# Kernel tuning notes

Measured on AMD Instinct MI355X. Metric: run time of the kernel, lower is better.

Reference implementation:

```python
import math
import jax, jax.numpy as jnp
import numpy as np

D = 512
H = 8
HD = D // H
FF = 2048
EPS = 1e-5


def _layernorm(x, gamma, beta):
    mean = jnp.mean(x, axis=-1, keepdims=True)
    var = jnp.mean((x - mean) ** 2, axis=-1, keepdims=True)
    return gamma * (x - mean) / jnp.sqrt(var + EPS) + beta


def _attention(q, k, v, mask):
    # q,k,v: [B,H,Sq/Sk,hd]; mask: [B,Sq,Sk] additive, broadcast over heads
    scale = 1.0 / math.sqrt(q.shape[-1])
    scores = jnp.einsum('bhqd,bhkd->bhqk', q, k) * scale
    scores = scores + mask[:, None, :, :]
    probs = jax.nn.softmax(scores, axis=-1)
    return jnp.einsum('bhqk,bhkd->bhqd', probs, v)


def setup_inputs() -> dict:
    key = jax.random.key(0)
    ks = jax.random.split(key, 20)
    B, S_ENC, S_DEC = 256, 512, 64
    s = 0.02
    inp = {
        'x': jax.random.normal(ks[0], (B, S_ENC, D), jnp.float32),
        'y': jax.random.normal(ks[1], (B, S_DEC, D), jnp.float32),
        'mask': jnp.zeros((B, S_DEC, S_DEC), jnp.float32),
        'mask2': jnp.zeros((B, S_DEC, S_ENC), jnp.float32),
        # self-attention params
        'qkv_w': jax.random.normal(ks[2], (D, 3 * D), jnp.float32) * s,
        'qkv_b': jnp.zeros((3 * D,), jnp.float32),
        'sa_out_w': jax.random.normal(ks[3], (D, D), jnp.float32) * s,
        'sa_out_b': jnp.zeros((D,), jnp.float32),
        # cross-attention params
        'q_w': jax.random.normal(ks[4], (D, D), jnp.float32) * s,
        'q_b': jnp.zeros((D,), jnp.float32),
        'kv_w': jax.random.normal(ks[5], (D, 2 * D), jnp.float32) * s,
        'kv_b': jnp.zeros((2 * D,), jnp.float32),
        'ca_out_w': jax.random.normal(ks[6], (D, D), jnp.float32) * s,
        'ca_out_b': jnp.zeros((D,), jnp.float32),
        # ffn params
        'l1_w': jax.random.normal(ks[7], (D, FF), jnp.float32) * s,
        'l1_b': jnp.zeros((FF,), jnp.float32),
        'l2_w': jax.random.normal(ks[8], (FF, D), jnp.float32) * s,
        'l2_b': jnp.zeros((D,), jnp.float32),
        # layernorm params
        'g1': jnp.ones((D,), jnp.float32), 'b1': jnp.zeros((D,), jnp.float32),
        'g2': jnp.ones((D,), jnp.float32), 'b2': jnp.zeros((D,), jnp.float32),
        'g3': jnp.ones((D,), jnp.float32), 'b3': jnp.zeros((D,), jnp.float32),
    }
    return inp


def reference(x, y, mask, mask2, qkv_w, qkv_b, sa_out_w, sa_out_b,
              q_w, q_b, kv_w, kv_b, ca_out_w, ca_out_b,
              l1_w, l1_b, l2_w, l2_b, g1, b1, g2, b2, g3, b3):
    B, Sd, _ = y.shape
    Se = x.shape[1]

    # --- self attention (post-norm, dropout is identity at eval) ---
    resid = y
    qkv = y @ qkv_w + qkv_b                     # [B,Sd,3D]
    qkv = qkv.reshape(B, Sd, H, 3 * HD).transpose(0, 2, 1, 3)
    q, k, v = jnp.split(qkv, 3, axis=-1)        # each [B,H,Sd,hd]
    vals = _attention(q, k, v, mask)
    vals = vals.transpose(0, 2, 1, 3).reshape(B, Sd, D)
    y = vals @ sa_out_w + sa_out_b
    y = _layernorm(y + resid, g1, b1)

    # --- cross attention: kv from encoder x, q from decoder y ---
    resid = y
    kv = x @ kv_w + kv_b                        # [B,Se,2D]
    kv = kv.reshape(B, Se, H, 2 * HD).transpose(0, 2, 1, 3)
    k, v = jnp.split(kv, 2, axis=-1)            # each [B,H,Se,hd]
    q = (y @ q_w + q_b).reshape(B, Sd, H, HD).transpose(0, 2, 1, 3)
    vals = _attention(q, k, v, mask2)
    vals = vals.transpose(0, 2, 1, 3).reshape(B, Sd, D)
    y = vals @ ca_out_w + ca_out_b
    y = _layernorm(y + resid, g2, b2)

    # --- feed forward ---
    resid = y
    h = jax.nn.relu(y @ l1_w + l1_b)
    y = h @ l2_w + l2_b
    y = _layernorm(y + resid, g3, b3)
    return y
```

## Files before the change

### kernel.cpp

```cpp
#include <hip/hip_runtime.h>
#include <hip/hip_bf16.h>
#include <stdint.h>


#define SDEC 64
#define SENC 512
#define DMODEL 512
#define FFDIM 2048

typedef __bf16 bf16x8 __attribute__((ext_vector_type(8)));
typedef float  f32x4  __attribute__((ext_vector_type(4)));

static __device__ __forceinline__ float bf2f(unsigned short u) {
  union { unsigned int i; float f; } w; w.i = ((unsigned int)u) << 16; return w.f;
}
static __device__ __forceinline__ unsigned short f2bf(float f) {
  union { float f; unsigned int i; } w; w.f = f;
  unsigned int u = w.i;
  return (unsigned short)((u + 0x7fffu + ((u >> 16) & 1u)) >> 16);
}

static __device__ __forceinline__ void gl_lds16(const unsigned short* g, unsigned short* l) {
  __builtin_amdgcn_global_load_lds(
      (const __attribute__((address_space(1))) unsigned int*)g,
      (__attribute__((address_space(3))) unsigned int*)l,
      16, 0, 0);
}

__global__ __launch_bounds__(256)
void cvt_f32_bf16(const float* __restrict__ in, unsigned short* __restrict__ out, size_t n8)
{
  size_t i = (size_t)blockIdx.x * blockDim.x + threadIdx.x;
  const size_t stride = (size_t)gridDim.x * blockDim.x;
  for (; i < n8; i += stride) {
    const float* p = in + i * 8;
    float4 a = *(const float4*)p, b = *(const float4*)(p + 4);
    union { unsigned short s[8]; uint4 v; } u;
    u.s[0] = f2bf(a.x); u.s[1] = f2bf(a.y); u.s[2] = f2bf(a.z); u.s[3] = f2bf(a.w);
    u.s[4] = f2bf(b.x); u.s[5] = f2bf(b.y); u.s[6] = f2bf(b.z); u.s[7] = f2bf(b.w);
    *(uint4*)(out + i * 8) = u.v;
  }
}

template<int RELU>
__global__ __launch_bounds__(256, 2)
void gemm_kernel(const unsigned short* __restrict__ A, const unsigned short* __restrict__ Bt,
                 const float* __restrict__ bias, unsigned short* __restrict__ C,
                 int M, int N, int K)
{
  __shared__ unsigned short sh[3 * 8192];
  const int tid = threadIdx.x;

  const int gx   = gridDim.x;
  const int nwg  = gx * gridDim.y;
  const int orig = blockIdx.y * gx + blockIdx.x;
  const int wg   = (orig & 7) * (nwg >> 3) + (orig >> 3);
  const int row0 = (wg / gx) * 128;
  const int col0 = (wg % gx) * 128;

  const int w = tid >> 6, lane = tid & 63;
  const int wm = w >> 1, wn = w & 1;
  const int gr = lane >> 2;
  const int gc = ((lane & 3) ^ ((lane >> 4) & 3)) * 8;

  auto STAGE = [&](int k0, int buf) {
    unsigned short* as = sh + buf * 8192;
    unsigned short* bs = as + 4096;
    #pragma unroll
    for (int i = 0; i < 2; ++i) {
      const int rbase = w * 32 + i * 16;
      gl_lds16(A  + (size_t)(row0 + rbase + gr) * K + (k0 + gc), as + rbase * 32);
      gl_lds16(Bt + (size_t)(col0 + rbase + gr) * K + (k0 + gc), bs + rbase * 32);
    }
  };

  f32x4 acc[4][4];
  #pragma unroll
  for (int i = 0; i < 4; ++i)
    #pragma unroll
    for (int j = 0; j < 4; ++j)
      acc[i][j] = (f32x4){0.f, 0.f, 0.f, 0.f};

  const int fr  = lane & 15;
  const int fks = ((lane >> 4) ^ (fr >> 2)) * 8;

  auto COMPUTE = [&](int buf) {
    const unsigned short* as = sh + buf * 8192;
    const unsigned short* bs = as + 4096;
    bf16x8 af[4], bfr[4];
    #pragma unroll
    for (int mi = 0; mi < 4; ++mi)
      af[mi] = *(const bf16x8*)&as[(wm * 64 + mi * 16 + fr) * 32 + fks];
    #pragma unroll
    for (int ni = 0; ni < 4; ++ni)
      bfr[ni] = *(const bf16x8*)&bs[(wn * 64 + ni * 16 + fr) * 32 + fks];
    __builtin_amdgcn_s_setprio(1);
    #pragma unroll
    for (int mi = 0; mi < 4; ++mi)
      #pragma unroll
      for (int ni = 0; ni < 4; ++ni)
        acc[mi][ni] = __builtin_amdgcn_mfma_f32_16x16x32_bf16(af[mi], bfr[ni], acc[mi][ni], 0, 0, 0);
    __builtin_amdgcn_s_setprio(0);
  };

  const int NT = K >> 5;
  STAGE(0, 0);
  STAGE(32, 1);
  int bc = 0, bn = 2;
  for (int t = 0; t < NT - 2; ++t) {
    STAGE((t + 2) << 5, bn);
    asm volatile("s_waitcnt vmcnt(8)" ::: "memory");
    __builtin_amdgcn_s_barrier();
    asm volatile("" ::: "memory");
    COMPUTE(bc);
    asm volatile("" ::: "memory");
    __builtin_amdgcn_s_barrier();
    bc = (bc + 1 == 3) ? 0 : bc + 1;
    bn = (bn + 1 == 3) ? 0 : bn + 1;
  }
  asm volatile("s_waitcnt vmcnt(4)" ::: "memory");
  __builtin_amdgcn_s_barrier();
  asm volatile("" ::: "memory");
  COMPUTE(bc);
  asm volatile("" ::: "memory");
  __builtin_amdgcn_s_barrier();
  bc = (bc + 1 == 3) ? 0 : bc + 1;
  asm volatile("s_waitcnt vmcnt(0)" ::: "memory");
  __builtin_amdgcn_s_barrier();
  asm volatile("" ::: "memory");
  COMPUTE(bc);
  asm volatile("" ::: "memory");
  __builtin_amdgcn_s_barrier();

  {
    const int fq = lane >> 4;
    #pragma unroll
    for (int ni = 0; ni < 4; ++ni) {
      const int c = wn * 64 + ni * 16 + fr;
      const float bv = bias ? bias[col0 + c] : 0.f;
      #pragma unroll
      for (int mi = 0; mi < 4; ++mi) {
        #pragma unroll
        for (int t = 0; t < 4; ++t) {
          const int r = wm * 64 + mi * 16 + fq * 4 + t;
          float v = acc[mi][ni][t] + bv;
          if (RELU) v = fmaxf(v, 0.f);
          sh[r * 128 + c] = f2bf(v);
        }
      }
    }
    __syncthreads();
    const int rr = tid >> 4;
    const int cc = (tid & 15) * 8;
    #pragma unroll
    for (int p = 0; p < 8; ++p) {
      const int r = p * 16 + rr;
      *(uint4*)(C + (size_t)(row0 + r) * N + col0 + cc) = *(const uint4*)&sh[r * 128 + cc];
    }
  }
}

__global__ __launch_bounds__(256, 2)
void attn_mfma(const unsigned short* __restrict__ qbuf, int qstride, int qmul,
               const unsigned short* __restrict__ kvbuf, int kvstride, int kmul, int kadd,
               int tokmul, int Skv, const float* __restrict__ mask,
               unsigned short* __restrict__ vals, float scale)
{
  __shared__ unsigned short Qs[64 * 72];
  __shared__ unsigned short Ks[64 * 72];
  __shared__ unsigned short Vt[64 * 72];
  __shared__ unsigned short Ps[64 * 72];

  const int nwg  = gridDim.x * gridDim.y;
  const int orig = blockIdx.y * gridDim.x + blockIdx.x;
  const int wg   = (orig & 7) * (nwg >> 3) + (orig >> 3);
  const int h = wg & 7, b = wg >> 3;

  const int tid = threadIdx.x;
  const int w = tid >> 6, lane = tid & 63;
  const int srow = tid >> 2;
  const int sc0 = (tid & 3) * 16;

  {
    const unsigned short* qg = qbuf + (size_t)(b * 64 + srow) * qstride + h * qmul + sc0;
    *(uint4*)&Qs[srow * 72 + sc0]     = *(const uint4*)qg;
    *(uint4*)&Qs[srow * 72 + sc0 + 8] = *(const uint4*)(qg + 8);
  }

  const int fr = lane & 15;
  const int fg = lane >> 4;
  const int orow = fg * 4;

  float mstate[4], lstate[4];
  f32x4 oacc[4];
  #pragma unroll
  for (int t = 0; t < 4; ++t) { mstate[t] = -1e30f; lstate[t] = 0.f; }
  #pragma unroll
  for (int ni = 0; ni < 4; ++ni) oacc[ni] = (f32x4){0.f, 0.f, 0.f, 0.f};

  for (int j0 = 0; j0 < Skv; j0 += 64) {
    __syncthreads();
    {
      const unsigned short* kg = kvbuf + (size_t)(b * tokmul + j0 + srow) * kvstride
                                 + h * kmul + kadd + sc0;
      *(uint4*)&Ks[srow * 72 + sc0]     = *(const uint4*)kg;
      *(uint4*)&Ks[srow * 72 + sc0 + 8] = *(const uint4*)(kg + 8);
      const unsigned short* vg = kg + 64;
      uint4 v0 = *(const uint4*)vg;
      uint4 v1 = *(const uint4*)(vg + 8);
      const unsigned short* vsp = (const unsigned short*)&v0;
      #pragma unroll
      for (int jj = 0; jj < 8; ++jj) Vt[(sc0 + jj) * 72 + srow] = vsp[jj];
      vsp = (const unsigned short*)&v1;
      #pragma unroll
      for (int jj = 0; jj < 8; ++jj) Vt[(sc0 + 8 + jj) * 72 + srow] = vsp[jj];
    }
    __syncthreads();

    f32x4 s[4];
    #pragma unroll
    for (int ni = 0; ni < 4; ++ni) s[ni] = (f32x4){0.f, 0.f, 0.f, 0.f};
    #pragma unroll
    for (int ks = 0; ks < 2; ++ks) {
      bf16x8 aq = *(const bf16x8*)&Qs[(w * 16 + fr) * 72 + ks * 32 + fg * 8];
      #pragma unroll
      for (int ni = 0; ni < 4; ++ni) {
        bf16x8 bk = *(const bf16x8*)&Ks[(ni * 16 + fr) * 72 + ks * 32 + fg * 8];
        s[ni] = __builtin_amdgcn_mfma_f32_16x16x32_bf16(aq, bk, s[ni], 0, 0, 0);
      }
    }

    #pragma unroll
    for (int t = 0; t < 4; ++t) {
      const int grow = w * 16 + orow + t;
      const float* mrow = mask + ((size_t)b * 64 + grow) * Skv + j0;
      float sv[4];
      float tmax = -1e30f;
      #pragma unroll
      for (int ni = 0; ni < 4; ++ni) {
        sv[ni] = s[ni][t] * scale + mrow[ni * 16 + fr];
        tmax = fmaxf(tmax, sv[ni]);
      }
      #pragma unroll
      for (int off = 1; off < 16; off <<= 1) tmax = fmaxf(tmax, __shfl_xor(tmax, off));
      const float mn = fmaxf(mstate[t], tmax);
      const float fscl = __expf(mstate[t] - mn);
      mstate[t] = mn;
      float psum = 0.f;
      #pragma unroll
      for (int ni = 0; ni < 4; ++ni) {
        float p = __expf(sv[ni] - mn);
        psum += p;
        Ps[grow * 72 + ni * 16 + fr] = f2bf(p);
      }
      #pragma unroll
      for (int off = 1; off < 16; off <<= 1) psum += __shfl_xor(psum, off);
      lstate[t] = lstate[t] * fscl + psum;
      #pragma unroll
      for (int ni = 0; ni < 4; ++ni) oacc[ni][t] *= fscl;
    }
    __syncthreads();

    #pragma unroll
    for (int ks = 0; ks < 2; ++ks) {
      bf16x8 pa = *(const bf16x8*)&Ps[(w * 16 + fr) * 72 + ks * 32 + fg * 8];
      #pragma unroll
      for (int ni = 0; ni < 4; ++ni) {
        bf16x8 vb = *(const bf16x8*)&Vt[(ni * 16 + fr) * 72 + ks * 32 + fg * 8];
        oacc[ni] = __builtin_amdgcn_mfma_f32_16x16x32_bf16(pa, vb, oacc[ni], 0, 0, 0);
      }
    }
  }

  #pragma unroll
  for (int t = 0; t < 4; ++t) {
    const int grow = w * 16 + orow + t;
    const float inv = 1.f / lstate[t];
    unsigned short* og = vals + (size_t)(b * 64 + grow) * DMODEL + h * 64;
    #pragma unroll
    for (int ni = 0; ni < 4; ++ni)
      og[ni * 16 + fr] = f2bf(oacc[ni][t] * inv);
  }
}

__global__ __launch_bounds__(256)
void ln_kernel(const unsigned short* __restrict__ proj16, const float* __restrict__ resid32,
               const unsigned short* __restrict__ resid16,
               const float* __restrict__ gamma, const float* __restrict__ beta,
               unsigned short* __restrict__ out16, float* __restrict__ out32)
{
  const int w = threadIdx.x >> 6, lane = threadIdx.x & 63;
  const size_t r = (size_t)blockIdx.x * 4 + w;
  const int d0 = lane * 8;

  float x[8];
  {
    uint4 u = *(const uint4*)(proj16 + r * DMODEL + d0);
    const unsigned short* s = (const unsigned short*)&u;
    #pragma unroll
    for (int j = 0; j < 8; ++j) x[j] = bf2f(s[j]);
  }
  if (resid32) {
    const float* p = resid32 + r * DMODEL + d0;
    float4 a = *(const float4*)p, b = *(const float4*)(p + 4);
    x[0] += a.x; x[1] += a.y; x[2] += a.z; x[3] += a.w;
    x[4] += b.x; x[5] += b.y; x[6] += b.z; x[7] += b.w;
  } else {
    uint4 u = *(const uint4*)(resid16 + r * DMODEL + d0);
    const unsigned short* s = (const unsigned short*)&u;
    #pragma unroll
    for (int j = 0; j < 8; ++j) x[j] += bf2f(s[j]);
  }

  float sum = 0.f;
  #pragma unroll
  for (int j = 0; j < 8; ++j) sum += x[j];
  #pragma unroll
  for (int off = 32; off > 0; off >>= 1) sum += __shfl_xor(sum, off);
  const float mean = sum * (1.f / DMODEL);

  float vs = 0.f;
  #pragma unroll
  for (int j = 0; j < 8; ++j) { float t = x[j] - mean; vs += t * t; }
  #pragma unroll
  for (int off = 32; off > 0; off >>= 1) vs += __shfl_xor(vs, off);
  const float rstd = rsqrtf(vs * (1.f / DMODEL) + 1e-5f);

  float4 g0 = *(const float4*)(gamma + d0), g1 = *(const float4*)(gamma + d0 + 4);
  float4 b0 = *(const float4*)(beta + d0),  b1 = *(const float4*)(beta + d0 + 4);
  const float g[8]  = {g0.x, g0.y, g0.z, g0.w, g1.x, g1.y, g1.z, g1.w};
  const float bb[8] = {b0.x, b0.y, b0.z, b0.w, b1.x, b1.y, b1.z, b1.w};
  float y[8];
  #pragma unroll
  for (int j = 0; j < 8; ++j) y[j] = g[j] * (x[j] - mean) * rstd + bb[j];

  if (out16) {
    union { unsigned short s[8]; uint4 v; } p;
    #pragma unroll
    for (int j = 0; j < 8; ++j) p.s[j] = f2bf(y[j]);
    *(uint4*)(out16 + r * DMODEL + d0) = p.v;
  }
  if (out32) {
    float* o = out32 + r * DMODEL + d0;
    *(float4*)o       = (float4){y[0], y[1], y[2], y[3]};
    *(float4*)(o + 4) = (float4){y[4], y[5], y[6], y[7]};
  }
}

__global__ __launch_bounds__(256)
void transpose_cvt(const float* __restrict__ W, unsigned short* __restrict__ Wt,
                   int K, int N)
{
  __shared__ float tile[32][33];
  const int tx = threadIdx.x, ty = threadIdx.y;
  const int n = blockIdx.x * 32 + tx;
  #pragma unroll
  for (int rr = 0; rr < 4; ++rr) {
    const int k = blockIdx.y * 32 + ty + rr * 8;
    tile[ty + rr * 8][tx] = W[(size_t)k * N + n];
  }
  __syncthreads();
  const int k2 = blockIdx.y * 32 + tx;
  #pragma unroll
  for (int rr = 0; rr < 4; ++rr) {
    const int n2 = blockIdx.x * 32 + ty + rr * 8;
    Wt[(size_t)n2 * K + k2] = f2bf(tile[tx][ty + rr * 8]);
  }
}

extern "C" void kernel_launch(void* const* d_in, const int* in_sizes, int n_in,
                              void* d_out, int out_size, void* d_ws, size_t ws_size,
                              hipStream_t stream)
{
  const float* x        = (const float*)d_in[0];
  const float* y        = (const float*)d_in[1];
  const float* mask     = (const float*)d_in[2];
  const float* mask2    = (const float*)d_in[3];
  const float* qkv_w    = (const float*)d_in[4];
  const float* qkv_b    = (const float*)d_in[5];
  const float* sa_out_w = (const float*)d_in[6];
  const float* sa_out_b = (const float*)d_in[7];
  const float* q_w      = (const float*)d_in[8];
  const float* q_b      = (const float*)d_in[9];
  const float* kv_w     = (const float*)d_in[10];
  const float* kv_b     = (const float*)d_in[11];
  const float* ca_out_w = (const float*)d_in[12];
  const float* ca_out_b = (const float*)d_in[13];
  const float* l1_w     = (const float*)d_in[14];
  const float* l1_b     = (const float*)d_in[15];
  const float* l2_w     = (const float*)d_in[16];
  const float* l2_b     = (const float*)d_in[17];
  const float* g1 = (const float*)d_in[18];
  const float* b1 = (const float*)d_in[19];
  const float* g2 = (const float*)d_in[20];
  const float* b2 = (const float*)d_in[21];
  const float* g3 = (const float*)d_in[22];
  const float* b3 = (const float*)d_in[23];

  const int B  = in_sizes[1] / (SDEC * DMODEL);
  const int M  = B * SDEC;
  const int ME = B * SENC;

  char* ws = (char*)d_ws;
  size_t off = 0;
  auto alloc = [&](size_t bytes) -> char* {
    char* p = ws + off;
    off += (bytes + 255) & ~(size_t)255;
    return p;
  };
  unsigned short* qkv_wt = (unsigned short*)alloc((size_t)1536 * 512 * 2);
  unsigned short* sa_wt  = (unsigned short*)alloc((size_t)512 * 512 * 2);
  unsigned short* q_wt   = (unsigned short*)alloc((size_t)512 * 512 * 2);
  unsigned short* kv_wt  = (unsigned short*)alloc((size_t)1024 * 512 * 2);
  unsigned short* ca_wt  = (unsigned short*)alloc((size_t)512 * 512 * 2);
  unsigned short* l1_wt  = (unsigned short*)alloc((size_t)2048 * 512 * 2);
  unsigned short* l2_wt  = (unsigned short*)alloc((size_t)512 * 2048 * 2);
  unsigned short* kvb    = (unsigned short*)alloc((size_t)ME * 1024 * 2);
  char*           xreg   = alloc((size_t)ME * 512 * 2);
  unsigned short* xb     = (unsigned short*)xreg;
  unsigned short* qkvb   = (unsigned short*)xreg;
  unsigned short* qb     = (unsigned short*)xreg;
  unsigned short* y2b    = (unsigned short*)(xreg + (size_t)16777216);
  unsigned short* valsb  = (unsigned short*)(xreg + (size_t)50331648);
  unsigned short* proj   = (unsigned short*)(xreg + (size_t)67108864);
  unsigned short* y1b    = (unsigned short*)(xreg + (size_t)100663296);
  unsigned short* yb     = (unsigned short*)(xreg + (size_t)117440512);
  unsigned short* hb     = kvb;
  (void)ws_size; (void)n_in; (void)out_size;

  dim3 tb(32, 8);
  transpose_cvt<<<dim3(1536 / 32, 512 / 32), tb, 0, stream>>>(qkv_w, qkv_wt, 512, 1536);
  transpose_cvt<<<dim3(512 / 32, 512 / 32), tb, 0, stream>>>(sa_out_w, sa_wt, 512, 512);
  transpose_cvt<<<dim3(512 / 32, 512 / 32), tb, 0, stream>>>(q_w, q_wt, 512, 512);
  transpose_cvt<<<dim3(1024 / 32, 512 / 32), tb, 0, stream>>>(kv_w, kv_wt, 512, 1024);
  transpose_cvt<<<dim3(512 / 32, 512 / 32), tb, 0, stream>>>(ca_out_w, ca_wt, 512, 512);
  transpose_cvt<<<dim3(2048 / 32, 512 / 32), tb, 0, stream>>>(l1_w, l1_wt, 512, 2048);
  transpose_cvt<<<dim3(512 / 32, 2048 / 32), tb, 0, stream>>>(l2_w, l2_wt, 2048, 512);

  const float scale = 0.125f;

  cvt_f32_bf16<<<4096, 256, 0, stream>>>(x, xb, (size_t)ME * 512 / 8);
  gemm_kernel<0><<<dim3(1024 / 128, ME / 128), 256, 0, stream>>>(xb, kv_wt, kv_b, kvb, ME, 1024, 512);

  cvt_f32_bf16<<<4096, 256, 0, stream>>>(y, yb, (size_t)M * 512 / 8);
  gemm_kernel<0><<<dim3(1536 / 128, M / 128), 256, 0, stream>>>(yb, qkv_wt, qkv_b, qkvb, M, 1536, 512);
  attn_mfma<<<dim3(8, B), 256, 0, stream>>>(qkvb, 1536, 192, qkvb, 1536, 192, 64, SDEC, SDEC, mask, valsb, scale);
  gemm_kernel<0><<<dim3(512 / 128, M / 128), 256, 0, stream>>>(valsb, sa_wt, sa_out_b, proj, M, 512, 512);
  ln_kernel<<<M / 4, 256, 0, stream>>>(proj, y, nullptr, g1, b1, y1b, nullptr);

  gemm_kernel<0><<<dim3(512 / 128, M / 128), 256, 0, stream>>>(y1b, q_wt, q_b, qb, M, 512, 512);
  attn_mfma<<<dim3(8, B), 256, 0, stream>>>(qb, 512, 64, kvb, 1024, 128, 0, SENC, SENC, mask2, valsb, scale);
  gemm_kernel<0><<<dim3(512 / 128, M / 128), 256, 0, stream>>>(valsb, ca_wt, ca_out_b, proj, M, 512, 512);
  ln_kernel<<<M / 4, 256, 0, stream>>>(proj, nullptr, y1b, g2, b2, y2b, nullptr);

  gemm_kernel<1><<<dim3(2048 / 128, M / 128), 256, 0, stream>>>(y2b, l1_wt, l1_b, hb, M, 2048, 512);
  gemm_kernel<0><<<dim3(512 / 128, M / 128), 256, 0, stream>>>(hb, l2_wt, l2_b, proj, M, 512, 2048);
  ln_kernel<<<M / 4, 256, 0, stream>>>(proj, nullptr, y2b, g3, b3, nullptr, (float*)d_out);
}
```

Baseline: 628.4 us.

## Fuse fp32-to-bf16 input conversion into GEMM A-tile loading, double-buffer GEMM

Removes the separate fp32→bf16 conversion kernels for the encoder and decoder inputs. A new GEMM variant loads fp32 A tiles into registers, converts them and writes them to LDS, double-buffered against async B loads. The existing GEMM also drops from triple to double buffering and loses its swizzled LDS layout and setprio, while the epilogue gains an XOR swizzle. This saves a full read/write pass over the 64M-element x tensor but may add LDS bank conflicts and reduce latency hiding in the main GEMMs.

Result: no change. 638.7 us (+1.6%).

```diff
diff --git a/kernel.cpp b/kernel.cpp
--- a/kernel.cpp
+++ b/kernel.cpp
@@ -27,20 +27,53 @@
       16, 0, 0);
 }
 
-__global__ __launch_bounds__(256)
-void cvt_f32_bf16(const float* __restrict__ in, unsigned short* __restrict__ out, size_t n8)
-{
-  size_t i = (size_t)blockIdx.x * blockDim.x + threadIdx.x;
-  const size_t stride = (size_t)gridDim.x * blockDim.x;
-  for (; i < n8; i += stride) {
-    const float* p = in + i * 8;
-    float4 a = *(const float4*)p, b = *(const float4*)(p + 4);
-    union { unsigned short s[8]; uint4 v; } u;
-    u.s[0] = f2bf(a.x); u.s[1] = f2bf(a.y); u.s[2] = f2bf(a.z); u.s[3] = f2bf(a.w);
-    u.s[4] = f2bf(b.x); u.s[5] = f2bf(b.y); u.s[6] = f2bf(b.z); u.s[7] = f2bf(b.w);
-    *(uint4*)(out + i * 8) = u.v;
-  }
-}
+#define GEMM_COMPUTE(asrc, bsrc)                                                     \
+  {                                                                                  \
+    const unsigned short* as_ = (asrc);                                              \
+    const unsigned short* bs_ = (bsrc);                                              \
+    bf16x8 af[4], bfr[4];                                                            \
+    _Pragma("unroll")                                                                \
+    for (int mi = 0; mi < 4; ++mi)                                                   \
+      af[mi] = *(const bf16x8*)&as_[(wm * 64 + mi * 16 + fr) * 32 + fk];             \
+    _Pragma("unroll")                                                                \
+    for (int ni = 0; ni < 4; ++ni)                                                   \
+      bfr[ni] = *(const bf16x8*)&bs_[(wn * 64 + ni * 16 + fr) * 32 + fk];            \
+    _Pragma("unroll")                                                                \
+    for (int mi = 0; mi < 4; ++mi)                                                   \
+      _Pragma("unroll")                                                              \
+      for (int ni = 0; ni < 4; ++ni)                                                 \
+        acc[mi][ni] = __builtin_amdgcn_mfma_f32_16x16x32_bf16(af[mi], bfr[ni],       \
+                                                              acc[mi][ni], 0, 0, 0); \
+  }
+
+#define GEMM_EPILOGUE(RELU_)                                                          \
+  {                                                                                   \
+    const int fq = lane >> 4;                                                         \
+    _Pragma("unroll")                                                                 \
+    for (int ni = 0; ni < 4; ++ni) {                                                  \
+      const int c = wn * 64 + ni * 16 + fr;                                           \
+      const float bv = bias ? bias[col0 + c] : 0.f;                                   \
+      _Pragma("unroll")                                                               \
+      for (int mi = 0; mi < 4; ++mi) {                                                \
+        _Pragma("unroll")                                                             \
+        for (int t = 0; t < 4; ++t) {                                                 \
+          const int r = wm * 64 + mi * 16 + fq * 4 + t;                               \
+          float v = acc[mi][ni][t] + bv;                                              \
+          if (RELU_) v = fmaxf(v, 0.f);                                               \
+          sh[r * 128 + (c ^ (fq << 4))] = f2bf(v);           \
+        }                                                                             \
+      }                                                                               \
+    }                                                                                 \
+    __syncthreads();                                                                  \
+    const int rr = tid >> 4;                \
+    const int cc = (tid & 15) * 8;                                                    \
+    _Pragma("unroll")                                                                 \
+    for (int p = 0; p < 8; ++p) {                                                     \
+      const int r = p * 16 + rr;                                                      \
+      *(uint4*)(C + (size_t)(row0 + r) * N + col0 + cc) =                             \
+          *(const uint4*)&sh[r * 128 + (cc ^ (w << 4))];                              \
+    }                                                                                 \
+  }
 
 template<int RELU>
 __global__ __launch_bounds__(256, 2)
@@ -48,7 +81,7 @@
                  const float* __restrict__ bias, unsigned short* __restrict__ C,
                  int M, int N, int K)
 {
-  __shared__ unsigned short sh[3 * 8192];
+  __shared__ unsigned short sh[2 * 8192];
   const int tid = threadIdx.x;
 
   const int gx   = gridDim.x;
@@ -60,8 +93,7 @@
 
   const int w = tid >> 6, lane = tid & 63;
   const int wm = w >> 1, wn = w & 1;
-  const int gr = lane >> 2;
-  const int gc = ((lane & 3) ^ ((lane >> 4) & 3)) * 8;
+  const int gr = lane >> 2, gc = (lane & 3) * 8;
 
   auto STAGE = [&](int k0, int buf) {
     unsigned short* as = sh + buf * 8192;
@@ -81,83 +113,130 @@
     for (int j = 0; j < 4; ++j)
       acc[i][j] = (f32x4){0.f, 0.f, 0.f, 0.f};
 
-  const int fr  = lane & 15;
-  const int fks = ((lane >> 4) ^ (fr >> 2)) * 8;
-
-  auto COMPUTE = [&](int buf) {
-    const unsigned short* as = sh + buf * 8192;
-    const unsigned short* bs = as + 4096;
-    bf16x8 af[4], bfr[4];
-    #pragma unroll
-    for (int mi = 0; mi < 4; ++mi)
-      af[mi] = *(const bf16x8*)&as[(wm * 64 + mi * 16 + fr) * 32 + fks];
-    #pragma unroll
-    for (int ni = 0; ni < 4; ++ni)
-      bfr[ni] = *(const bf16x8*)&bs[(wn * 64 + ni * 16 + fr) * 32 + fks];
-    __builtin_amdgcn_s_setprio(1);
-    #pragma unroll
-    for (int mi = 0; mi < 4; ++mi)
-      #pragma unroll
-      for (int ni = 0; ni < 4; ++ni)
-        acc[mi][ni] = __builtin_amdgcn_mfma_f32_16x16x32_bf16(af[mi], bfr[ni], acc[mi][ni], 0, 0, 0);
-    __builtin_amdgcn_s_setprio(0);
-  };
-
-  const int NT = K >> 5;
+  const int fr = lane & 15, fk = (lane >> 4) * 8;
+
   STAGE(0, 0);
-  STAGE(32, 1);
-  int bc = 0, bn = 2;
-  for (int t = 0; t < NT - 2; ++t) {
-    STAGE((t + 2) << 5, bn);
-    asm volatile("s_waitcnt vmcnt(8)" ::: "memory");
+  int cur = 0;
+  for (int k0 = 0; k0 + 32 < K; k0 += 32) {
+    STAGE(k0 + 32, cur ^ 1);
+    asm volatile("s_waitcnt vmcnt(4)" ::: "memory");
     __builtin_amdgcn_s_barrier();
     asm volatile("" ::: "memory");
-    COMPUTE(bc);
+    GEMM_COMPUTE(sh + cur * 8192, sh + cur * 8192 + 4096);
     asm volatile("" ::: "memory");
     __builtin_amdgcn_s_barrier();
-    bc = (bc + 1 == 3) ? 0 : bc + 1;
-    bn = (bn + 1 == 3) ? 0 : bn + 1;
-  }
-  asm volatile("s_waitcnt vmcnt(4)" ::: "memory");
-  __builtin_amdgcn_s_barrier();
-  asm volatile("" ::: "memory");
-  COMPUTE(bc);
-  asm volatile("" ::: "memory");
-  __builtin_amdgcn_s_barrier();
-  bc = (bc + 1 == 3) ? 0 : bc + 1;
+    cur ^= 1;
+  }
   asm volatile("s_waitcnt vmcnt(0)" ::: "memory");
   __builtin_amdgcn_s_barrier();
   asm volatile("" ::: "memory");
-  COMPUTE(bc);
+  GEMM_COMPUTE(sh + cur * 8192, sh + cur * 8192 + 4096);
   asm volatile("" ::: "memory");
   __builtin_amdgcn_s_barrier();
 
-  {
-    const int fq = lane >> 4;
-    #pragma unroll
-    for (int ni = 0; ni < 4; ++ni) {
-      const int c = wn * 64 + ni * 16 + fr;
-      const float bv = bias ? bias[col0 + c] : 0.f;
-      #pragma unroll
-      for (int mi = 0; mi < 4; ++mi) {
-        #pragma unroll
-        for (int t = 0; t < 4; ++t) {
-          const int r = wm * 64 + mi * 16 + fq * 4 + t;
-          float v = acc[mi][ni][t] + bv;
-          if (RELU) v = fmaxf(v, 0.f);
-          sh[r * 128 + c] = f2bf(v);
-        }
+  GEMM_EPILOGUE(RELU);
+}
+
+template<int RELU>
+__global__ __launch_bounds__(256, 2)
+void gemm_a32_kernel(const float* __restrict__ A, const unsigned short* __restrict__ Bt,
+                     const float* __restrict__ bias, unsigned short* __restrict__ C,
+                     int M, int N, int K)
+{
+  __shared__ unsigned short sh[2 * 8192];
+  const int tid = threadIdx.x;
+
+  const int gx   = gridDim.x;
+  const int nwg  = gx * gridDim.y;
+  const int orig = blockIdx.y * gx + blockIdx.x;
+  const int wg   = (orig & 7) * (nwg >> 3) + (orig >> 3);
+  const int row0 = (wg / gx) * 128;
+  const int col0 = (wg % gx) * 128;
+
+  const int w = tid >> 6, lane = tid & 63;
+  const int wm = w >> 1, wn = w & 1;
+  const int gr = lane >> 2, gc = (lane & 3) * 8;
+  const int srow = tid >> 2;
+  const int scol = (tid & 3) * 8;
+
+  auto STAGE_B = [&](int t, int buf) {
+    unsigned short* bs = sh + buf * 8192 + 4096;
+    #pragma unroll
+    for (int i = 0; i < 2; ++i) {
+      const int rbase = w * 32 + i * 16;
+      gl_lds16(Bt + (size_t)(col0 + rbase + gr) * K + (t * 32 + gc), bs + rbase * 32);
+    }
+  };
+  auto LOAD_A = [&](int t, f32x4& o0, f32x4& o1, f32x4& o2, f32x4& o3) {
+    const float* p0 = A + (size_t)(row0 + srow) * K + t * 32 + scol;
+    const float* p1 = A + (size_t)(row0 + srow + 64) * K + t * 32 + scol;
+    asm volatile("global_load_dwordx4 %0, %1, off"           : "=&v"(o0) : "v"(p0));
+    asm volatile("global_load_dwordx4 %0, %1, off offset:16" : "=&v"(o1) : "v"(p0));
+    asm volatile("global_load_dwordx4 %0, %1, off"           : "=&v"(o2) : "v"(p1));
+    asm volatile("global_load_dwordx4 %0, %1, off offset:16" : "=&v"(o3) : "v"(p1));
+  };
+  auto WRITE_A = [&](const f32x4& a0, const f32x4& a1, const f32x4& a2, const f32x4& a3,
+                     int buf) {
+    unsigned short* as = sh + buf * 8192;
+    union { unsigned short s[8]; uint4 v; } p;
+    #pragma unroll
+    for (int j = 0; j < 4; ++j) { p.s[j] = f2bf(a0[j]); p.s[4 + j] = f2bf(a1[j]); }
+    *(uint4*)&as[srow * 32 + scol] = p.v;
+    #pragma unroll
+    for (int j = 0; j < 4; ++j) { p.s[j] = f2bf(a2[j]); p.s[4 + j] = f2bf(a3[j]); }
+    *(uint4*)&as[(srow + 64) * 32 + scol] = p.v;
+  };
+
+  f32x4 acc[4][4];
+  #pragma unroll
+  for (int i = 0; i < 4; ++i)
+    #pragma unroll
+    for (int j = 0; j < 4; ++j)
+      acc[i][j] = (f32x4){0.f, 0.f, 0.f, 0.f};
+
+  const int fr = lane & 15, fk = (lane >> 4) * 8;
+
+  f32x4 ra0, ra1, ra2, ra3, rb0, rb1, rb2, rb3;
+
+  STAGE_B(0, 0);
+  LOAD_A(0, ra0, ra1, ra2, ra3);
+
+  const int NT = K >> 5;
+  for (int tt = 0; tt < NT; tt += 2) {
+    {
+      STAGE_B(tt + 1, 1);
+      LOAD_A(tt + 1, rb0, rb1, rb2, rb3);
+      asm volatile("s_waitcnt vmcnt(6)" ::: "memory");
+      __builtin_amdgcn_sched_barrier(0);
+      WRITE_A(ra0, ra1, ra2, ra3, 0);
+      asm volatile("s_waitcnt lgkmcnt(0)" ::: "memory");
+      __builtin_amdgcn_sched_barrier(0);
+      __builtin_amdgcn_s_barrier();
+      GEMM_COMPUTE(sh, sh + 4096);
+      asm volatile("" ::: "memory");
+      __builtin_amdgcn_s_barrier();
+    }
+    {
+      const bool pref = (tt + 2) < NT;
+      if (pref) {
+        STAGE_B(tt + 2, 0);
+        LOAD_A(tt + 2, ra0, ra1, ra2, ra3);
+        asm volatile("s_waitcnt vmcnt(6)" ::: "memory");
+      } else {
+        asm volatile("s_waitcnt vmcnt(0)" ::: "memory");
       }
-    }
-    __syncthreads();
-    const int rr = tid >> 4;
-    const int cc = (tid & 15) * 8;
-    #pragma unroll
-    for (int p = 0; p < 8; ++p) {
-      const int r = p * 16 + rr;
-      *(uint4*)(C + (size_t)(row0 + r) * N + col0 + cc) = *(const uint4*)&sh[r * 128 + cc];
-    }
-  }
+      __builtin_amdgcn_sched_barrier(0);
+      WRITE_A(rb0, rb1, rb2, rb3, 1);
+      asm volatile("s_waitcnt lgkmcnt(0)" ::: "memory");
+      __builtin_amdgcn_sched_barrier(0);
+      __builtin_amdgcn_s_barrier();
+      GEMM_COMPUTE(sh + 8192, sh + 8192 + 4096);
+      asm volatile("" ::: "memory");
+      __builtin_amdgcn_s_barrier();
+    }
+  }
+
+  GEMM_EPILOGUE(RELU);
 }
 
 __global__ __launch_bounds__(256, 2)
@@ -417,14 +496,12 @@
   unsigned short* l2_wt  = (unsigned short*)alloc((size_t)512 * 2048 * 2);
   unsigned short* kvb    = (unsigned short*)alloc((size_t)ME * 1024 * 2);
   char*           xreg   = alloc((size_t)ME * 512 * 2);
-  unsigned short* xb     = (unsigned short*)xreg;
   unsigned short* qkvb   = (unsigned short*)xreg;
   unsigned short* qb     = (unsigned short*)xreg;
   unsigned short* y2b    = (unsigned short*)(xreg + (size_t)16777216);
   unsigned short* valsb  = (unsigned short*)(xreg + (size_t)50331648);
   unsigned short* proj   = (unsigned short*)(xreg + (size_t)67108864);
   unsigned short* y1b    = (unsigned short*)(xreg + (size_t)100663296);
-  unsigned short* yb     = (unsigned short*)(xreg + (size_t)117440512);
   unsigned short* hb     = kvb;
   (void)ws_size; (void)n_in; (void)out_size;
 
@@ -439,11 +516,9 @@
 
   const float scale = 0.125f;
 
-  cvt_f32_bf16<<<4096, 256, 0, stream>>>(x, xb, (size_t)ME * 512 / 8);
-  gemm_kernel<0><<<dim3(1024 / 128, ME / 128), 256, 0, stream>>>(xb, kv_wt, kv_b, kvb, ME, 1024, 512);
-
-  cvt_f32_bf16<<<4096, 256, 0, stream>>>(y, yb, (size_t)M * 512 / 8);
-  gemm_kernel<0><<<dim3(1536 / 128, M / 128), 256, 0, stream>>>(yb, qkv_wt, qkv_b, qkvb, M, 1536, 512);
+  gemm_a32_kernel<0><<<dim3(1024 / 128, ME / 128), 256, 0, stream>>>(x, kv_wt, kv_b, kvb, ME, 1024, 512);
+
+  gemm_a32_kernel<0><<<dim3(1536 / 128, M / 128), 256, 0, stream>>>(y, qkv_wt, qkv_b, qkvb, M, 1536, 512);
   attn_mfma<<<dim3(8, B), 256, 0, stream>>>(qkvb, 1536, 192, qkvb, 1536, 192, 64, SDEC, SDEC, mask, valsb, scale);
   gemm_kernel<0><<<dim3(512 / 128, M / 128), 256, 0, stream>>>(valsb, sa_wt, sa_out_b, proj, M, 512, 512);
   ln_kernel<<<M / 4, 256, 0, stream>>>(proj, y, nullptr, g1, b1, y1b, nullptr);
```

## Switch GEMM to double-buffered LDS with new swizzles for loads and epilogue

Applied to the files above, without the earlier changes.

Replaces the GEMM's three-stage LDS ring buffer with a two-stage ping-pong buffer, which cuts shared memory per block from 48 KB to 32 KB. It also changes the XOR swizzle for A/B tiles to key on pairs of rows, adds an XOR swizzle to the epilogue staging to reduce LDS bank conflicts, and drops the s_setprio hints around the MFMA block. The trade-off is a shallower prefetch depth, so global load latency may be less hidden, in exchange for less LDS pressure and fewer bank conflicts.

Result: faster. 607.0 us (-3.4%).

```diff
diff --git a/kernel.cpp b/kernel.cpp
--- a/kernel.cpp
+++ b/kernel.cpp
@@ -42,13 +42,32 @@
   }
 }
 
+#define GEMM_COMPUTE(asrc, bsrc)                                                     \
+  {                                                                                  \
+    const unsigned short* as_ = (asrc);                                              \
+    const unsigned short* bs_ = (bsrc);                                              \
+    bf16x8 af[4], bfr[4];                                                            \
+    _Pragma("unroll")                                                                \
+    for (int mi = 0; mi < 4; ++mi)                                                   \
+      af[mi] = *(const bf16x8*)&as_[(wm * 64 + mi * 16 + fr) * 32 + fsw];            \
+    _Pragma("unroll")                                                                \
+    for (int ni = 0; ni < 4; ++ni)                                                   \
+      bfr[ni] = *(const bf16x8*)&bs_[(wn * 64 + ni * 16 + fr) * 32 + fsw];           \
+    _Pragma("unroll")                                                                \
+    for (int mi = 0; mi < 4; ++mi)                                                   \
+      _Pragma("unroll")                                                              \
+      for (int ni = 0; ni < 4; ++ni)                                                 \
+        acc[mi][ni] = __builtin_amdgcn_mfma_f32_16x16x32_bf16(af[mi], bfr[ni],       \
+                                                              acc[mi][ni], 0, 0, 0); \
+  }
+
 template<int RELU>
 __global__ __launch_bounds__(256, 2)
 void gemm_kernel(const unsigned short* __restrict__ A, const unsigned short* __restrict__ Bt,
                  const float* __restrict__ bias, unsigned short* __restrict__ C,
                  int M, int N, int K)
 {
-  __shared__ unsigned short sh[3 * 8192];
+  __shared__ unsigned short sh[2 * 8192];
   const int tid = threadIdx.x;
 
   const int gx   = gridDim.x;
@@ -61,7 +80,7 @@
   const int w = tid >> 6, lane = tid & 63;
   const int wm = w >> 1, wn = w & 1;
   const int gr = lane >> 2;
-  const int gc = ((lane & 3) ^ ((lane >> 4) & 3)) * 8;
+  const int gc = ((lane & 3) ^ ((lane >> 3) & 3)) * 8;
 
   auto STAGE = [&](int k0, int buf) {
     unsigned short* as = sh + buf * 8192;
@@ -82,53 +101,25 @@
       acc[i][j] = (f32x4){0.f, 0.f, 0.f, 0.f};
 
   const int fr  = lane & 15;
-  const int fks = ((lane >> 4) ^ (fr >> 2)) * 8;
-
-  auto COMPUTE = [&](int buf) {
-    const unsigned short* as = sh + buf * 8192;
-    const unsigned short* bs = as + 4096;
-    bf16x8 af[4], bfr[4];
-    #pragma unroll
-    for (int mi = 0; mi < 4; ++mi)
-      af[mi] = *(const bf16x8*)&as[(wm * 64 + mi * 16 + fr) * 32 + fks];
-    #pragma unroll
-    for (int ni = 0; ni < 4; ++ni)
-      bfr[ni] = *(const bf16x8*)&bs[(wn * 64 + ni * 16 + fr) * 32 + fks];
-    __builtin_amdgcn_s_setprio(1);
-    #pragma unroll
-    for (int mi = 0; mi < 4; ++mi)
-      #pragma unroll
-      for (int ni = 0; ni < 4; ++ni)
-        acc[mi][ni] = __builtin_amdgcn_mfma_f32_16x16x32_bf16(af[mi], bfr[ni], acc[mi][ni], 0, 0, 0);
-    __builtin_amdgcn_s_setprio(0);
-  };
-
-  const int NT = K >> 5;
+  const int fg  = lane >> 4;
+  const int fsw = (fg ^ ((fr >> 1) & 3)) * 8;
+
   STAGE(0, 0);
-  STAGE(32, 1);
-  int bc = 0, bn = 2;
-  for (int t = 0; t < NT - 2; ++t) {
-    STAGE((t + 2) << 5, bn);
-    asm volatile("s_waitcnt vmcnt(8)" ::: "memory");
+  int cur = 0;
+  for (int k0 = 0; k0 + 32 < K; k0 += 32) {
+    STAGE(k0 + 32, cur ^ 1);
+    asm volatile("s_waitcnt vmcnt(4)" ::: "memory");
     __builtin_amdgcn_s_barrier();
     asm volatile("" ::: "memory");
-    COMPUTE(bc);
+    GEMM_COMPUTE(sh + cur * 8192, sh + cur * 8192 + 4096);
     asm volatile("" ::: "memory");
     __builtin_amdgcn_s_barrier();
-    bc = (bc + 1 == 3) ? 0 : bc + 1;
-    bn = (bn + 1 == 3) ? 0 : bn + 1;
-  }
-  asm volatile("s_waitcnt vmcnt(4)" ::: "memory");
-  __builtin_amdgcn_s_barrier();
-  asm volatile("" ::: "memory");
-  COMPUTE(bc);
-  asm volatile("" ::: "memory");
-  __builtin_amdgcn_s_barrier();
-  bc = (bc + 1 == 3) ? 0 : bc + 1;
+    cur ^= 1;
+  }
   asm volatile("s_waitcnt vmcnt(0)" ::: "memory");
   __builtin_amdgcn_s_barrier();
   asm volatile("" ::: "memory");
-  COMPUTE(bc);
+  GEMM_COMPUTE(sh + cur * 8192, sh + cur * 8192 + 4096);
   asm volatile("" ::: "memory");
   __builtin_amdgcn_s_barrier();
 
@@ -145,7 +136,7 @@
           const int r = wm * 64 + mi * 16 + fq * 4 + t;
           float v = acc[mi][ni][t] + bv;
           if (RELU) v = fmaxf(v, 0.f);
-          sh[r * 128 + c] = f2bf(v);
+          sh[r * 128 + (c ^ (fq << 4))] = f2bf(v);
         }
       }
     }
@@ -155,7 +146,8 @@
     #pragma unroll
     for (int p = 0; p < 8; ++p) {
       const int r = p * 16 + rr;
-      *(uint4*)(C + (size_t)(row0 + r) * N + col0 + cc) = *(const uint4*)&sh[r * 128 + cc];
+      *(uint4*)(C + (size_t)(row0 + r) * N + col0 + cc) =
+          *(const uint4*)&sh[r * 128 + (cc ^ (w << 4))];
     }
   }
 }
```
